# Optimization experiments

Measured on AMD Instinct MI355X. Metric: run time of the kernel, lower is better.

## Reference

```python
import jax, jax.numpy as jnp
import numpy as np

B, L_TXT, L_IMG = 1, 256, 2048
D_MODEL, HEADS, DIM_HEAD = 2048, 16, 128
S = L_TXT + L_IMG
QMAX = 127.0  # int8 symmetric
SM_SCALE = 1.0 / float(np.sqrt(DIM_HEAD))


def quant_act(x):
    # dynamic per-tensor symmetric int8 fake-quant with straight-through estimator
    scale = jnp.maximum(jnp.max(jnp.abs(x)) / QMAX, 1e-8)
    q = jnp.clip(jnp.round(x / scale), -QMAX, QMAX) * scale
    return x + jax.lax.stop_gradient(q - x)


def quant_weight(w):
    # per-output-channel symmetric int8 fake-quant (STE)
    scale = jnp.maximum(jnp.max(jnp.abs(w), axis=1, keepdims=True) / QMAX, 1e-8)
    q = jnp.clip(jnp.round(w / scale), -QMAX, QMAX) * scale
    return w + jax.lax.stop_gradient(q - w)


def qlinear(x, w, b):
    return x @ quant_weight(w).T + b


def rmsnorm(x, w, eps=1e-6):
    var = jnp.mean(jnp.square(x), axis=-1, keepdims=True)
    return x * jax.lax.rsqrt(var + eps) * w


def apply_rope(x, cos, sin):
    # diffusers apply_rotary_emb, use_real with interleaved (real, imag) pairs
    xr = x.reshape(*x.shape[:-1], -1, 2)
    rot = jnp.stack([-xr[..., 1], xr[..., 0]], axis=-1).reshape(x.shape)
    return x * cos + rot * sin


def heads_split(x):
    # [B, L, H*D] -> [B, H, L, D]
    return x.reshape(B, -1, HEADS, DIM_HEAD).transpose(0, 2, 1, 3)


def setup_inputs() -> dict:
    key = jax.random.key(0)
    ks = jax.random.split(key, 12)
    inp = {
        'hidden_states': jax.random.normal(ks[0], (B, L_IMG, D_MODEL), jnp.float32),
        'encoder_hidden_states': jax.random.normal(ks[1], (B, L_TXT, D_MODEL), jnp.float32),
    }
    freqs = 1.0 / (10000.0 ** (jnp.arange(0, DIM_HEAD, 2, dtype=jnp.float32) / DIM_HEAD))
    ang = jnp.arange(S, dtype=jnp.float32)[:, None] * freqs[None, :]  # [S, D/2]
    inp['rope_cos'] = jnp.repeat(jnp.cos(ang), 2, axis=-1)  # [S, D]
    inp['rope_sin'] = jnp.repeat(jnp.sin(ang), 2, axis=-1)
    wn = ['wq', 'wk', 'wv', 'w_add_q', 'w_add_k', 'w_add_v', 'w_out', 'w_add_out']
    bn = ['bq', 'bk', 'bv', 'b_add_q', 'b_add_k', 'b_add_v', 'b_out', 'b_add_out']
    for i, (w, b) in enumerate(zip(wn, bn)):
        inp[w] = jax.random.normal(ks[2 + i], (D_MODEL, D_MODEL), jnp.float32) * 0.02
        inp[b] = jnp.zeros((D_MODEL,), jnp.float32)
    for n in ['norm_q_w', 'norm_k_w', 'norm_added_q_w', 'norm_added_k_w']:
        inp[n] = jnp.ones((DIM_HEAD,), jnp.float32)
    return inp


def reference(hidden_states, encoder_hidden_states, rope_cos, rope_sin,
              wq, bq, wk, bk, wv, bv,
              w_add_q, b_add_q, w_add_k, b_add_k, w_add_v, b_add_v,
              w_out, b_out, w_add_out, b_add_out,
              norm_q_w, norm_k_w, norm_added_q_w, norm_added_k_w):
    # image-token branch
    h = quant_act(hidden_states)
    q = heads_split(qlinear(h, wq, bq))
    k = heads_split(qlinear(h, wk, bk))
    v = heads_split(qlinear(h, wv, bv))
    q = quant_act(rmsnorm(q, norm_q_w))
    k = quant_act(rmsnorm(k, norm_k_w))
    v = quant_act(v)
    # text-token (encoder) branch
    e = quant_act(encoder_hidden_states)
    eq = heads_split(qlinear(e, w_add_q, b_add_q))
    ek = heads_split(qlinear(e, w_add_k, b_add_k))
    ev = heads_split(qlinear(e, w_add_v, b_add_v))
    eq = quant_act(rmsnorm(eq, norm_added_q_w))
    ek = quant_act(rmsnorm(ek, norm_added_k_w))
    ev = quant_act(ev)
    # joint sequence: [text; image]
    q = jnp.concatenate([eq, q], axis=2)
    k = jnp.concatenate([ek, k], axis=2)
    v = jnp.concatenate([ev, v], axis=2)
    cos = rope_cos[None, None]
    sin = rope_sin[None, None]
    q = apply_rope(q, cos, sin)
    k = apply_rope(k, cos, sin)
    scores = jnp.einsum('bhqd,bhkd->bhqk', q, k) * SM_SCALE
    probs = jax.nn.softmax(scores, axis=-1)
    out = jnp.einsum('bhqk,bhkd->bhqd', probs, v)
    out = out.transpose(0, 2, 1, 3).reshape(B, S, HEADS * DIM_HEAD)
    out = quant_act(out)
    enc, img = out[:, :L_TXT], out[:, L_TXT:]
    img = qlinear(img, w_out, b_out)
    enc = qlinear(enc, w_add_out, b_add_out)
    return (img, enc)
```

## Files before the change

kernel.cpp:

```cpp
#include <hip/hip_runtime.h>

constexpr int L_TXT = 256, L_IMG = 2048, SEQ = 2304;
constexpr int DM = 2048, NH = 16, DH = 128;
constexpr int NSPLIT = 4;
constexpr int SSTR = 32;

typedef __attribute__((ext_vector_type(8))) __bf16 bf16x8;
typedef __attribute__((ext_vector_type(4))) float f32x4;

__device__ __forceinline__ float ldin(const void* p, size_t i, int bf) {
  return bf ? (float)((const __bf16*)p)[i] : ((const float*)p)[i];
}
__device__ __forceinline__ float slot_scale(const unsigned* s) {
  return fmaxf(__uint_as_float(*s) / 127.0f, 1e-8f);
}
__device__ __forceinline__ float qclamp(float x, float sc) {
  float q = rintf(x / sc);
  return fminf(fmaxf(q, -127.0f), 127.0f);
}
__device__ __forceinline__ float block_allmax_n(float v) {
  #pragma unroll
  for (int off = 32; off; off >>= 1) v = fmaxf(v, __shfl_xor(v, off));
  __shared__ float sm[16];
  int nw = blockDim.x >> 6;
  __syncthreads();
  if ((threadIdx.x & 63) == 0) sm[threadIdx.x >> 6] = v;
  __syncthreads();
  float m = sm[0];
  for (int i = 1; i < nw; i++) m = fmaxf(m, sm[i]);
  return m;
}

__global__ void detect_k(const void* cosp, int* flag) {
  if (threadIdx.x == 0) *flag = (((const unsigned short*)cosp)[0] != 0) ? 1 : 0;
}

struct Ptrs8 { const void* p[8]; };

__global__ void quant_weights_k(Ptrs8 win, __bf16* __restrict__ wq, float* __restrict__ scales,
                                const int* __restrict__ flagp) {
  const int bf = *flagp;
  int row = blockIdx.x, mat = blockIdx.y, t = threadIdx.x;
  float v[8];
  if (bf) {
    union { int4 q; __bf16 h[8]; } u;
    u.q = ((const int4*)((const __bf16*)win.p[mat] + (size_t)row * DM))[t];
    #pragma unroll
    for (int j = 0; j < 8; j++) v[j] = (float)u.h[j];
  } else {
    const float4* p = (const float4*)((const float*)win.p[mat] + (size_t)row * DM);
    float4 a = p[t * 2], b = p[t * 2 + 1];
    v[0]=a.x; v[1]=a.y; v[2]=a.z; v[3]=a.w; v[4]=b.x; v[5]=b.y; v[6]=b.z; v[7]=b.w;
  }
  float m = 0.f;
  #pragma unroll
  for (int j = 0; j < 8; j++) m = fmaxf(m, fabsf(v[j]));
  m = block_allmax_n(m);
  float sc = fmaxf(m / 127.0f, 1e-8f);
  if (t == 0) scales[mat * DM + row] = sc;
  union { int4 q; __bf16 h[8]; } o;
  #pragma unroll
  for (int j = 0; j < 8; j++) o.h[j] = (__bf16)qclamp(v[j], sc);
  ((int4*)(wq + (size_t)mat * DM * DM + (size_t)row * DM))[t] = o.q;
}
__global__ void weight_scales_k(Ptrs8 win, float* __restrict__ scales, const int* __restrict__ flagp) {
  const int bf = *flagp;
  int row = blockIdx.x, mat = blockIdx.y, t = threadIdx.x;
  float m = 0.f;
  for (int c = t; c < DM; c += 256) m = fmaxf(m, fabsf(ldin(win.p[mat], (size_t)row * DM + c, bf)));
  m = block_allmax_n(m);
  if (t == 0) scales[mat * DM + row] = fmaxf(m / 127.0f, 1e-8f);
}

__global__ void absmax_he_k(const void* __restrict__ hs, const void* __restrict__ es,
                            unsigned* s0, unsigned* s1, const int* __restrict__ flagp) {
  const int bf = *flagp;
  const int n18 = L_IMG * DM / 8, n28 = L_TXT * DM / 8;
  float m1 = 0.f, m2 = 0.f;
  for (int i = blockIdx.x * 256 + threadIdx.x; i < n18 + n28; i += gridDim.x * 256) {
    bool h = i < n18;
    const void* src = h ? hs : es;
    int j = h ? i : i - n18;
    float lm = 0.f;
    if (bf) {
      union { int4 q; __bf16 x[8]; } u; u.q = ((const int4*)src)[j];
      #pragma unroll
      for (int k = 0; k < 8; k++) lm = fmaxf(lm, fabsf((float)u.x[k]));
    } else {
      const float4* p = (const float4*)src;
      float4 a = p[j * 2], b = p[j * 2 + 1];
      lm = fmaxf(fmaxf(fmaxf(fabsf(a.x), fabsf(a.y)), fmaxf(fabsf(a.z), fabsf(a.w))),
                 fmaxf(fmaxf(fabsf(b.x), fabsf(b.y)), fmaxf(fabsf(b.z), fabsf(b.w))));
    }
    if (h) m1 = fmaxf(m1, lm); else m2 = fmaxf(m2, lm);
  }
  m1 = block_allmax_n(m1);
  __syncthreads();
  m2 = block_allmax_n(m2);
  if (threadIdx.x == 0) { atomicMax(s0, __float_as_uint(m1)); atomicMax(s1, __float_as_uint(m2)); }
}

__global__ void quant_he_k(const void* __restrict__ hs, const void* __restrict__ es,
                           const unsigned* __restrict__ slots, __bf16* __restrict__ hqo,
                           __bf16* __restrict__ eqo, const int* __restrict__ flagp) {
  const int bf = *flagp;
  const int n18 = L_IMG * DM / 8, n28 = L_TXT * DM / 8;
  float sc0 = slot_scale(slots), sc1 = slot_scale(slots + SSTR);
  for (int i = blockIdx.x * 256 + threadIdx.x; i < n18 + n28; i += gridDim.x * 256) {
    bool h = i < n18;
    const void* src = h ? hs : es;
    int j = h ? i : i - n18;
    float sc = h ? sc0 : sc1;
    float v[8];
    if (bf) {
      union { int4 q; __bf16 x[8]; } u; u.q = ((const int4*)src)[j];
      #pragma unroll
      for (int k = 0; k < 8; k++) v[k] = (float)u.x[k];
    } else {
      const float4* p = (const float4*)src;
      float4 a = p[j * 2], b = p[j * 2 + 1];
      v[0]=a.x; v[1]=a.y; v[2]=a.z; v[3]=a.w; v[4]=b.x; v[5]=b.y; v[6]=b.z; v[7]=b.w;
    }
    union { int4 q; __bf16 x[8]; } o;
    #pragma unroll
    for (int k = 0; k < 8; k++) o.x[k] = (__bf16)qclamp(v[k], sc);
    ((int4*)(h ? hqo : eqo))[j] = o.q;
  }
}

__global__ void quant_f32x8_k(const float* __restrict__ x, int n8,
                              const unsigned* __restrict__ slot, __bf16* __restrict__ out) {
  float sc = slot_scale(slot);
  for (int i = blockIdx.x * 256 + threadIdx.x; i < n8; i += gridDim.x * 256) {
    float4 a = ((const float4*)x)[i * 2], b = ((const float4*)x)[i * 2 + 1];
    union { int4 q; __bf16 h[8]; } o;
    o.h[0]=(__bf16)qclamp(a.x,sc); o.h[1]=(__bf16)qclamp(a.y,sc);
    o.h[2]=(__bf16)qclamp(a.z,sc); o.h[3]=(__bf16)qclamp(a.w,sc);
    o.h[4]=(__bf16)qclamp(b.x,sc); o.h[5]=(__bf16)qclamp(b.y,sc);
    o.h[6]=(__bf16)qclamp(b.z,sc); o.h[7]=(__bf16)qclamp(b.w,sc);
    ((int4*)out)[i] = o.q;
  }
}
__global__ void absmax_f32_k(const float* __restrict__ x, int n, unsigned* slot) {
  float m = 0.f;
  for (int i = blockIdx.x * 256 + threadIdx.x; i < n; i += gridDim.x * 256)
    m = fmaxf(m, fabsf(x[i]));
  m = block_allmax_n(m);
  if (threadIdx.x == 0) atomicMax(slot, __float_as_uint(m));
}

__global__ void rms_absmax_v_k(float* __restrict__ qf, float* __restrict__ kf, float* __restrict__ vf,
                               const void* nq, const void* naq, const void* nk, const void* nak,
                               unsigned* __restrict__ slots, const int* __restrict__ flagp) {
  const int bf = *flagp;
  const int t = threadIdx.x, lane = t & 63, wave = t >> 6;
  float wqt0 = ldin(naq, lane, bf), wqt1 = ldin(naq, lane + 64, bf);
  float wqi0 = ldin(nq,  lane, bf), wqi1 = ldin(nq,  lane + 64, bf);
  float wkt0 = ldin(nak, lane, bf), wkt1 = ldin(nak, lane + 64, bf);
  float wki0 = ldin(nk,  lane, bf), wki1 = ldin(nk,  lane + 64, bf);
  const int NR = NH * SEQ;
  float mx[6] = {0.f, 0.f, 0.f, 0.f, 0.f, 0.f};
  for (int row = blockIdx.x * 16 + wave; row < 3 * NR; row += gridDim.x * 16) {
    int tns = row / NR, r2 = row - tns * NR;
    int s = r2 % SEQ; bool txt = s < L_TXT;
    float* p = (tns == 0 ? qf : tns == 1 ? kf : vf) + (size_t)r2 * DH;
    float v0 = p[lane], v1 = p[lane + 64];
    if (tns < 2) {
      float ss = v0 * v0 + v1 * v1;
      #pragma unroll
      for (int off = 32; off; off >>= 1) ss += __shfl_xor(ss, off);
      float r = rsqrtf(ss * (1.0f / 128.0f) + 1e-6f);
      float w0, w1;
      if (tns == 0) { w0 = txt ? wqt0 : wqi0; w1 = txt ? wqt1 : wqi1; }
      else          { w0 = txt ? wkt0 : wki0; w1 = txt ? wkt1 : wki1; }
      v0 *= r * w0; v1 *= r * w1;
      p[lane] = v0; p[lane + 64] = v1;
    }
    int idx = tns * 2 + (txt ? 0 : 1);
    mx[idx] = fmaxf(mx[idx], fmaxf(fabsf(v0), fabsf(v1)));
  }
  #pragma unroll
  for (int off = 32; off; off >>= 1)
    #pragma unroll
    for (int j = 0; j < 6; j++) mx[j] = fmaxf(mx[j], __shfl_xor(mx[j], off));
  __shared__ float smx[16][6];
  if (lane == 0)
    #pragma unroll
    for (int j = 0; j < 6; j++) smx[wave][j] = mx[j];
  __syncthreads();
  if (t == 0) {
    #pragma unroll
    for (int j = 0; j < 6; j++) {
      float m = smx[0][j];
      for (int i = 1; i < 16; i++) m = fmaxf(m, smx[i][j]);
      atomicMax(slots + (2 + j) * SSTR, __float_as_uint(m));
    }
  }
}

__global__ void rope2_k(const float* __restrict__ qf, const float* __restrict__ kf,
                        const void* cosb, const void* sinb, const unsigned* __restrict__ slots,
                        __bf16* __restrict__ qb, __bf16* __restrict__ kb, const int* __restrict__ flagp) {
  const int bf = *flagp;
  const int NP = NH * SEQ * 64;
  for (int i = blockIdx.x * 256 + threadIdx.x; i < 2 * NP; i += gridDim.x * 256) {
    int tns = i >= NP;
    int j = i - tns * NP;
    int pr = j & 63, rowg = j >> 6;
    int s = rowg % SEQ;
    const float* src = tns ? kf : qf;
    __bf16* dst = tns ? kb : qb;
    float sc = slot_scale(slots + (tns ? 4 : 2) * SSTR + (s < L_TXT ? 0 : SSTR));
    size_t base = (size_t)rowg * DH + pr * 2;
    float2 x2 = *(const float2*)(src + base);
    float q0 = qclamp(x2.x, sc) * sc, q1 = qclamp(x2.y, sc) * sc;
    float c0 = ldin(cosb, s * DH + 2 * pr, bf), c1 = ldin(cosb, s * DH + 2 * pr + 1, bf);
    float s0 = ldin(sinb, s * DH + 2 * pr, bf), s1 = ldin(sinb, s * DH + 2 * pr + 1, bf);
    dst[base]     = (__bf16)(q0 * c0 - q1 * s0);
    dst[base + 1] = (__bf16)(q1 * c1 + q0 * s1);
  }
}

__global__ void quant_transpose_v_k(const float* __restrict__ v, const unsigned* __restrict__ slots,
                                    __bf16* __restrict__ vt) {
  __shared__ float tile[64][65];
  int t = threadIdx.x;
  int s0 = blockIdx.x * 64, d0 = blockIdx.y * 64, h = blockIdx.z;
  #pragma unroll
  for (int i = 0; i < 16; i++) {
    int r = i * 4 + (t >> 6), c = t & 63;
    tile[r][c] = v[((size_t)(h * SEQ) + s0 + r) * DH + d0 + c];
  }
  __syncthreads();
  float sc = slot_scale(slots + (s0 < L_TXT ? 6 : 7) * SSTR);
  #pragma unroll
  for (int i = 0; i < 16; i++) {
    int d = i * 4 + (t >> 6), s = t & 63;
    float q = qclamp(tile[s][d], sc) * sc;
    vt[((size_t)(h * DH) + d0 + d) * SEQ + s0 + s] = (__bf16)q;
  }
}

struct GemmArgs {
  const __bf16 *hq, *eq, *attnq;
  const __bf16* wqp;
  const void* Wraw[8];
  const float* wsc;
  const void* bias[8];
  float* outs[3];
  void* dout;
  const unsigned* slots;
  const int* flagp;
};
template<int MODE, int QW>
__global__ __launch_bounds__(256, 2)
void gemm_f(GemmArgs a) {
  const int bf = *a.flagp;
  constexpr int K = DM;
  __shared__ __bf16 As[128][72];
  __shared__ __bf16 Ws[128][72];
  const int t = threadIdx.x, lane = t & 63, wave = t >> 6;
  const int l15 = lane & 15, quad = lane >> 4;
  const int n0 = blockIdx.x * 128, y = blockIdx.y;
  int mat, outrow; const __bf16* A; const unsigned* aslot;
  if (MODE == 0) {
    bool txt = y < 2;
    mat = blockIdx.z + (txt ? 3 : 0);
    A = (txt ? a.eq : a.hq) + (size_t)(txt ? y * 128 : (y - 2) * 128) * K;
    outrow = y * 128;
    aslot = a.slots + (txt ? SSTR : 0);
  } else {
    bool img = y < 16;
    mat = img ? 6 : 7;
    A = a.attnq + (size_t)(img ? L_TXT + y * 128 : (y - 16) * 128) * K;
    outrow = img ? y * 128 : L_IMG + (y - 16) * 128;
    aslot = a.slots + 8 * SSTR;
  }
  const __bf16* Wq = QW ? a.wqp + (size_t)mat * DM * DM : nullptr;
  const void* Wr = a.Wraw[mat];
  const float* wrow = a.wsc + mat * DM;
  int wm = (wave & 1) * 64, wn = (wave >> 1) * 64;
  f32x4 acc[4][4] = {};
  int sr = t >> 3, sc = (t & 7) * 8;
  float wsc4[4];
  if (!QW) {
    #pragma unroll
    for (int p = 0; p < 4; p++) wsc4[p] = wrow[n0 + p * 32 + sr];
  }
  for (int k0 = 0; k0 < K; k0 += 64) {
    __syncthreads();
    #pragma unroll
    for (int p = 0; p < 4; p++) {
      int r = p * 32 + sr;
      *(int4*)&As[r][sc] = *(const int4*)&A[(size_t)r * K + k0 + sc];
      if (QW) {
        *(int4*)&Ws[r][sc] = *(const int4*)&Wq[(size_t)(n0 + r) * K + k0 + sc];
      } else {
        union { bf16x8 v; __bf16 h[8]; } q;
        if (bf) {
          union { int4 v; __bf16 h[8]; } u;
          u.v = *(const int4*)((const __bf16*)Wr + (size_t)(n0 + r) * K + k0 + sc);
          #pragma unroll
          for (int j = 0; j < 8; j++) q.h[j] = (__bf16)qclamp((float)u.h[j], wsc4[p]);
        } else {
          const float* wp = (const float*)Wr + (size_t)(n0 + r) * K + k0 + sc;
          float4 x = *(const float4*)wp, z = *(const float4*)(wp + 4);
          q.h[0]=(__bf16)qclamp(x.x,wsc4[p]); q.h[1]=(__bf16)qclamp(x.y,wsc4[p]);
          q.h[2]=(__bf16)qclamp(x.z,wsc4[p]); q.h[3]=(__bf16)qclamp(x.w,wsc4[p]);
          q.h[4]=(__bf16)qclamp(z.x,wsc4[p]); q.h[5]=(__bf16)qclamp(z.y,wsc4[p]);
          q.h[6]=(__bf16)qclamp(z.z,wsc4[p]); q.h[7]=(__bf16)qclamp(z.w,wsc4[p]);
        }
        *(bf16x8*)&Ws[r][sc] = q.v;
      }
    }
    __syncthreads();
    #pragma unroll
    for (int kk = 0; kk < 64; kk += 32) {
      bf16x8 af[4], bfr[4];
      #pragma unroll
      for (int i = 0; i < 4; i++) {
        af[i]  = *(const bf16x8*)&As[wm + i * 16 + l15][kk + quad * 8];
        bfr[i] = *(const bf16x8*)&Ws[wn + i * 16 + l15][kk + quad * 8];
      }
      #pragma unroll
      for (int i = 0; i < 4; i++)
        #pragma unroll
        for (int j = 0; j < 4; j++)
          acc[i][j] = __builtin_amdgcn_mfma_f32_16x16x32_bf16(af[i], bfr[j], acc[i][j], 0, 0, 0);
    }
  }
  float asc = slot_scale(aslot);
  #pragma unroll
  for (int j = 0; j < 4; j++) {
    int gn = n0 + wn + j * 16 + l15;
    float wsb = wrow[gn] * asc;
    float bv = ldin(a.bias[mat], gn, bf);
    #pragma unroll
    for (int i = 0; i < 4; i++)
      #pragma unroll
      for (int r = 0; r < 4; r++) {
        int gm = wm + i * 16 + quad * 4 + r;
        float val = acc[i][j][r] * wsb + bv;
        if (MODE == 0) {
          a.outs[blockIdx.z][(size_t)(gn >> 7) * (SEQ * DH) + (size_t)(outrow + gm) * DH + (gn & 127)] = val;
        } else {
          size_t idx = (size_t)(outrow + gm) * DM + gn;
          if (bf) ((__bf16*)a.dout)[idx] = (__bf16)val; else ((float*)a.dout)[idx] = val;
        }
      }
  }
}

template<int SPLIT>
__global__ __launch_bounds__(256, 2)
void flash_attn_k(const __bf16* __restrict__ Qb, const __bf16* __restrict__ Kb,
                  const __bf16* __restrict__ Vt, float* __restrict__ O,
                  float* __restrict__ Op, float* __restrict__ Mp, float* __restrict__ Lp) {
  __shared__ __align__(16) char smem[19456 + 18432 + 18432];
  auto Ks = (__bf16(*)[152])smem;
  auto Vs = (__bf16(*)[72])(smem + 19456);
  auto Ps = (__bf16(*)[72])(smem + 19456 + 18432);
  const int t = threadIdx.x, lane = t & 63, wave = t >> 6;
  const int l15 = lane & 15, quad = lane >> 4;
  const int h = blockIdx.y, s0 = blockIdx.x * 128, qr = wave * 32;
  const float fscale = 0.08838834764831845f * 1.4426950408889634f;

  bf16x8 qf[2][4];
  #pragma unroll
  for (int mi = 0; mi < 2; mi++)
    #pragma unroll
    for (int kk = 0; kk < 4; kk++)
      qf[mi][kk] = *(const bf16x8*)&Qb[(size_t)(h * SEQ + s0 + qr + mi * 16 + l15) * DH + kk * 32 + quad * 8];

  f32x4 accO[2][8] = {};
  float m_st[2][4], l_st[2][4];
  #pragma unroll
  for (int mi = 0; mi < 2; mi++)
    #pragma unroll
    for (int r = 0; r < 4; r++) { m_st[mi][r] = -1e30f; l_st[mi][r] = 0.f; }

  const int ktb = SPLIT ? blockIdx.z * (SEQ / 64 / NSPLIT) : 0;
  const int kte = SPLIT ? ktb + (SEQ / 64 / NSPLIT) : SEQ / 64;

  const int krr = t >> 4, krc = (t & 15) * 8;
  const int vrr = t >> 3, vrc = (t & 7) * 8;
  int4 kreg[4], vreg[4];
  #pragma unroll
  for (int p = 0; p < 4; p++)
    kreg[p] = *(const int4*)&Kb[(size_t)(h * SEQ + ktb * 64 + p * 16 + krr) * DH + krc];
  #pragma unroll
  for (int p = 0; p < 4; p++)
    vreg[p] = *(const int4*)&Vt[(size_t)(h * DH + p * 32 + vrr) * SEQ + ktb * 64 + vrc];

  for (int kt = ktb; kt < kte; kt++) {
    asm volatile("s_waitcnt lgkmcnt(0)" ::: "memory");
    __builtin_amdgcn_s_barrier();
    #pragma unroll
    for (int p = 0; p < 4; p++) *(int4*)&Ks[p * 16 + krr][krc] = kreg[p];
    #pragma unroll
    for (int p = 0; p < 4; p++) *(int4*)&Vs[p * 32 + vrr][vrc] = vreg[p];
    if (kt + 1 < kte) {
      #pragma unroll
      for (int p = 0; p < 4; p++)
        kreg[p] = *(const int4*)&Kb[(size_t)(h * SEQ + (kt + 1) * 64 + p * 16 + krr) * DH + krc];
      #pragma unroll
      for (int p = 0; p < 4; p++)
        vreg[p] = *(const int4*)&Vt[(size_t)(h * DH + p * 32 + vrr) * SEQ + (kt + 1) * 64 + vrc];
    }
    asm volatile("s_waitcnt lgkmcnt(0)" ::: "memory");
    __builtin_amdgcn_s_barrier();

    f32x4 accS[2][4] = {};
    __builtin_amdgcn_s_setprio(1);
    #pragma unroll
    for (int kk = 0; kk < 4; kk++) {
      bf16x8 bk[4];
      #pragma unroll
      for (int ni = 0; ni < 4; ni++)
        bk[ni] = *(const bf16x8*)&Ks[ni * 16 + l15][kk * 32 + quad * 8];
      #pragma unroll
      for (int mi = 0; mi < 2; mi++)
        #pragma unroll
        for (int ni = 0; ni < 4; ni++)
          accS[mi][ni] = __builtin_amdgcn_mfma_f32_16x16x32_bf16(qf[mi][kk], bk[ni], accS[mi][ni], 0, 0, 0);
    }
    __builtin_amdgcn_s_setprio(0);

    float al[2][4];
    #pragma unroll
    for (int mi = 0; mi < 2; mi++)
      #pragma unroll
      for (int r = 0; r < 4; r++) {
        float rm = fmaxf(fmaxf(accS[mi][0][r], accS[mi][1][r]), fmaxf(accS[mi][2][r], accS[mi][3][r]));
        #pragma unroll
        for (int off = 8; off > 0; off >>= 1) rm = fmaxf(rm, __shfl_xor(rm, off));
        float mn = fmaxf(m_st[mi][r], rm);
        al[mi][r] = exp2f((m_st[mi][r] - mn) * fscale);
        m_st[mi][r] = mn;
      }
    #pragma unroll
    for (int mi = 0; mi < 2; mi++)
      #pragma unroll
      for (int r = 0; r < 4; r++) {
        float rs = 0.f;
        #pragma unroll
        for (int ni = 0; ni < 4; ni++) {
          float pv = exp2f((accS[mi][ni][r] - m_st[mi][r]) * fscale);
          accS[mi][ni][r] = pv;
          rs += pv;
        }
        #pragma unroll
        for (int off = 8; off > 0; off >>= 1) rs += __shfl_xor(rs, off);
        l_st[mi][r] = l_st[mi][r] * al[mi][r] + rs;
      }
    #pragma unroll
    for (int mi = 0; mi < 2; mi++)
      #pragma unroll
      for (int di = 0; di < 8; di++)
        #pragma unroll
        for (int r = 0; r < 4; r++)
          accO[mi][di][r] *= al[mi][r];
    #pragma unroll
    for (int mi = 0; mi < 2; mi++)
      #pragma unroll
      for (int ni = 0; ni < 4; ni++)
        #pragma unroll
        for (int r = 0; r < 4; r++)
          Ps[qr + mi * 16 + quad * 4 + r][ni * 16 + l15] = (__bf16)accS[mi][ni][r];
    __builtin_amdgcn_s_setprio(1);
    #pragma unroll
    for (int kk2 = 0; kk2 < 2; kk2++) {
      bf16x8 pa[2], vb[8];
      #pragma unroll
      for (int mi = 0; mi < 2; mi++)
        pa[mi] = *(const bf16x8*)&Ps[qr + mi * 16 + l15][kk2 * 32 + quad * 8];
      #pragma unroll
      for (int di = 0; di < 8; di++)
        vb[di] = *(const bf16x8*)&Vs[di * 16 + l15][kk2 * 32 + quad * 8];
      #pragma unroll
      for (int mi = 0; mi < 2; mi++)
        #pragma unroll
        for (int di = 0; di < 8; di++)
          accO[mi][di] = __builtin_amdgcn_mfma_f32_16x16x32_bf16(pa[mi], vb[di], accO[mi][di], 0, 0, 0);
    }
    __builtin_amdgcn_s_setprio(0);
  }
  if (SPLIT) {
    const size_t SP = (size_t)NH * SEQ * DH;
    const int sp = blockIdx.z;
    #pragma unroll
    for (int mi = 0; mi < 2; mi++)
      #pragma unroll
      for (int r = 0; r < 4; r++) {
        int gs = s0 + qr + mi * 16 + quad * 4 + r;
        size_t ib = sp * SP + ((size_t)h * SEQ + gs) * DH;
        if (l15 == 0) {
          Mp[(size_t)sp * NH * SEQ + h * SEQ + gs] = m_st[mi][r];
          Lp[(size_t)sp * NH * SEQ + h * SEQ + gs] = l_st[mi][r];
        }
        #pragma unroll
        for (int di = 0; di < 8; di++)
          Op[ib + di * 16 + l15] = accO[mi][di][r];
      }
  } else {
    #pragma unroll
    for (int mi = 0; mi < 2; mi++)
      #pragma unroll
      for (int r = 0; r < 4; r++) {
        float inv = 1.0f / l_st[mi][r];
        int gs = s0 + qr + mi * 16 + quad * 4 + r;
        #pragma unroll
        for (int di = 0; di < 8; di++)
          O[(size_t)gs * DM + h * DH + di * 16 + l15] = accO[mi][di][r] * inv;
      }
  }
}

__global__ void flash_combine_k(const float* __restrict__ Op, const float* __restrict__ Mp,
                                const float* __restrict__ Lp, float* __restrict__ O,
                                unsigned* __restrict__ slot8) {
  const float fscale = 0.08838834764831845f * 1.4426950408889634f;
  const int t = threadIdx.x, lane = t & 63, w = t >> 6;
  const size_t SP = (size_t)NH * SEQ * DH, MR = (size_t)NH * SEQ;
  float lm = 0.f;
  for (int row = blockIdx.x * 16 + w; row < NH * SEQ; row += gridDim.x * 16) {
    float m0 = Mp[row], m1 = Mp[MR + row], m2 = Mp[2 * MR + row], m3 = Mp[3 * MR + row];
    float M = fmaxf(fmaxf(m0, m1), fmaxf(m2, m3));
    float w0 = exp2f((m0 - M) * fscale), w1 = exp2f((m1 - M) * fscale);
    float w2 = exp2f((m2 - M) * fscale), w3 = exp2f((m3 - M) * fscale);
    float inv = 1.0f / (Lp[row] * w0 + Lp[MR + row] * w1 + Lp[2 * MR + row] * w2 + Lp[3 * MR + row] * w3);
    int h = row / SEQ, s = row % SEQ;
    size_t ob = (size_t)s * DM + h * DH, ib = (size_t)row * DH;
    #pragma unroll
    for (int j = 0; j < 2; j++) {
      int d = lane + j * 64;
      float v = (Op[ib + d] * w0 + Op[SP + ib + d] * w1 +
                 Op[2 * SP + ib + d] * w2 + Op[3 * SP + ib + d] * w3) * inv;
      O[ob + d] = v;
      lm = fmaxf(lm, fabsf(v));
    }
  }
  lm = block_allmax_n(lm);
  if (t == 0) atomicMax(slot8, __float_as_uint(lm));
}

extern "C" void kernel_launch(void* const* d_in, const int* in_sizes, int n_in,
                              void* d_out, int out_size, void* d_ws, size_t ws_size,
                              hipStream_t stream) {
  (void)in_sizes; (void)n_in; (void)out_size;
  const void* hs   = d_in[0];
  const void* es   = d_in[1];
  const void* cosb = d_in[2];
  const void* sinb = d_in[3];
  const void* W[8]; const void* Bv[8];
  for (int i = 0; i < 8; i++) { W[i] = d_in[4 + 2 * i]; Bv[i] = d_in[5 + 2 * i]; }
  const void* nq  = d_in[20];
  const void* nk  = d_in[21];
  const void* naq = d_in[22];
  const void* nak = d_in[23];

  char* ws = (char*)d_ws;
  size_t off = 0;
  auto take = [&](size_t b) { char* p = ws + off; off += (b + 255) & ~(size_t)255; return p; };
  const size_t T = (size_t)NH * SEQ * DH * 4;

  unsigned* slots = (unsigned*)take(16 * SSTR * 4);
  int* flagp = (int*)(slots + 15 * SSTR);
  float* wsc = (float*)take(8ull * DM * 4);

  size_t here = off;
  size_t need_base  = 4 * T + T + 3 * (T / 2) + 2 * ((size_t)NSPLIT * NH * SEQ * 4 + 256) + 1024;
  bool do_split = here + need_base <= ws_size;
  size_t region_sz = do_split ? 4 * T : 3 * T;

  char* region = take(region_sz);
  float* qf = (float*)region;
  float* kf = (float*)(region + T);
  float* vf = (float*)(region + 2 * T);
  float* Opart = (float*)region;
  __bf16* attnq = (__bf16*)region;
  char* attnfR = take(T);
  __bf16* hq = (__bf16*)attnfR;
  __bf16* eq = (__bf16*)(attnfR + (size_t)L_IMG * DM * 2);
  float* attnf = (float*)attnfR;
  __bf16* qb  = (__bf16*)take(T / 2);
  __bf16* kb  = (__bf16*)take(T / 2);
  __bf16* vtb = (__bf16*)take(T / 2);
  float* Mpart = (float*)take((size_t)NSPLIT * NH * SEQ * 4);
  float* Lpart = (float*)take((size_t)NSPLIT * NH * SEQ * 4);
  bool do_prequant = (off + 8ull * DM * DM * 2 + 256 <= ws_size);
  __bf16* wq = do_prequant ? (__bf16*)take(8ull * DM * DM * 2) : nullptr;

  hipMemsetAsync(slots, 0, 16 * SSTR * 4, stream);
  detect_k<<<1, 64, 0, stream>>>(cosb, flagp);

  Ptrs8 win;
  for (int i = 0; i < 8; i++) win.p[i] = W[i];
  if (do_prequant)
    quant_weights_k<<<dim3(DM, 8), 256, 0, stream>>>(win, wq, wsc, flagp);
  else
    weight_scales_k<<<dim3(DM, 8), 256, 0, stream>>>(win, wsc, flagp);

  absmax_he_k<<<512, 256, 0, stream>>>(hs, es, slots, slots + SSTR, flagp);
  quant_he_k<<<1024, 256, 0, stream>>>(hs, es, slots, hq, eq, flagp);

  GemmArgs ga;
  ga.hq = hq; ga.eq = eq; ga.attnq = attnq; ga.wqp = wq;
  for (int i = 0; i < 8; i++) { ga.Wraw[i] = W[i]; ga.bias[i] = Bv[i]; }
  ga.wsc = wsc; ga.outs[0] = qf; ga.outs[1] = kf; ga.outs[2] = vf;
  ga.dout = d_out; ga.slots = slots; ga.flagp = flagp;

  if (do_prequant)
    gemm_f<0, 1><<<dim3(16, 18, 3), 256, 0, stream>>>(ga);
  else
    gemm_f<0, 0><<<dim3(16, 18, 3), 256, 0, stream>>>(ga);

  rms_absmax_v_k<<<256, 1024, 0, stream>>>(qf, kf, vf, nq, naq, nk, nak, slots, flagp);
  rope2_k<<<1024, 256, 0, stream>>>(qf, kf, cosb, sinb, slots, qb, kb, flagp);
  quant_transpose_v_k<<<dim3(SEQ / 64, DH / 64, NH), 256, 0, stream>>>(vf, slots, vtb);

  if (do_split) {
    flash_attn_k<1><<<dim3(SEQ / 128, NH, NSPLIT), 256, 0, stream>>>(qb, kb, vtb, nullptr,
                                                                     Opart, Mpart, Lpart);
    flash_combine_k<<<288, 1024, 0, stream>>>(Opart, Mpart, Lpart, attnf, slots + 8 * SSTR);
  } else {
    flash_attn_k<0><<<dim3(SEQ / 128, NH), 256, 0, stream>>>(qb, kb, vtb, attnf,
                                                             nullptr, nullptr, nullptr);
    absmax_f32_k<<<256, 256, 0, stream>>>(attnf, SEQ * DM, slots + 8 * SSTR);
  }
  quant_f32x8_k<<<1024, 256, 0, stream>>>(attnf, SEQ * DM / 8, slots + 8 * SSTR, attnq);

  if (do_prequant)
    gemm_f<1, 1><<<dim3(16, 18), 256, 0, stream>>>(ga);
  else
    gemm_f<1, 0><<<dim3(16, 18), 256, 0, stream>>>(ga);
}
```

Measured before the change: 677.9 us.

## Shrink flash-attention query tile to 64 rows and alias P buffer onto K smem

```diff
diff --git a/kernel.cpp b/kernel.cpp
--- a/kernel.cpp
+++ b/kernel.cpp
@@ -352,32 +352,28 @@
 }
 
 template<int SPLIT>
-__global__ __launch_bounds__(256, 2)
+__global__ __launch_bounds__(256, 4)
 void flash_attn_k(const __bf16* __restrict__ Qb, const __bf16* __restrict__ Kb,
                   const __bf16* __restrict__ Vt, float* __restrict__ O,
                   float* __restrict__ Op, float* __restrict__ Mp, float* __restrict__ Lp) {
-  __shared__ __align__(16) char smem[19456 + 18432 + 18432];
+  __shared__ __align__(16) char smem[19456 + 18432];
   auto Ks = (__bf16(*)[152])smem;
   auto Vs = (__bf16(*)[72])(smem + 19456);
-  auto Ps = (__bf16(*)[72])(smem + 19456 + 18432);
+  auto Ps = (__bf16(*)[72])smem;
   const int t = threadIdx.x, lane = t & 63, wave = t >> 6;
   const int l15 = lane & 15, quad = lane >> 4;
-  const int h = blockIdx.y, s0 = blockIdx.x * 128, qr = wave * 32;
+  const int h = blockIdx.y, s0 = blockIdx.x * 64, qr = wave * 16;
   const float fscale = 0.08838834764831845f * 1.4426950408889634f;
 
-  bf16x8 qf[2][4];
-  #pragma unroll
-  for (int mi = 0; mi < 2; mi++)
-    #pragma unroll
-    for (int kk = 0; kk < 4; kk++)
-      qf[mi][kk] = *(const bf16x8*)&Qb[(size_t)(h * SEQ + s0 + qr + mi * 16 + l15) * DH + kk * 32 + quad * 8];
-
-  f32x4 accO[2][8] = {};
-  float m_st[2][4], l_st[2][4];
-  #pragma unroll
-  for (int mi = 0; mi < 2; mi++)
-    #pragma unroll
-    for (int r = 0; r < 4; r++) { m_st[mi][r] = -1e30f; l_st[mi][r] = 0.f; }
+  bf16x8 qf[4];
+  #pragma unroll
+  for (int kk = 0; kk < 4; kk++)
+    qf[kk] = *(const bf16x8*)&Qb[(size_t)(h * SEQ + s0 + qr + l15) * DH + kk * 32 + quad * 8];
+
+  f32x4 accO[8] = {};
+  float m_st[4], l_st[4];
+  #pragma unroll
+  for (int r = 0; r < 4; r++) { m_st[r] = -1e30f; l_st[r] = 0.f; }
 
   const int ktb = SPLIT ? blockIdx.z * (SEQ / 64 / NSPLIT) : 0;
   const int kte = SPLIT ? ktb + (SEQ / 64 / NSPLIT) : SEQ / 64;
@@ -410,78 +406,61 @@
     asm volatile("s_waitcnt lgkmcnt(0)" ::: "memory");
     __builtin_amdgcn_s_barrier();
 
-    f32x4 accS[2][4] = {};
+    f32x4 accS[4] = {};
     __builtin_amdgcn_s_setprio(1);
     #pragma unroll
-    for (int kk = 0; kk < 4; kk++) {
-      bf16x8 bk[4];
-      #pragma unroll
-      for (int ni = 0; ni < 4; ni++)
-        bk[ni] = *(const bf16x8*)&Ks[ni * 16 + l15][kk * 32 + quad * 8];
-      #pragma unroll
-      for (int mi = 0; mi < 2; mi++)
-        #pragma unroll
-        for (int ni = 0; ni < 4; ni++)
-          accS[mi][ni] = __builtin_amdgcn_mfma_f32_16x16x32_bf16(qf[mi][kk], bk[ni], accS[mi][ni], 0, 0, 0);
-    }
+    for (int kk = 0; kk < 4; kk++)
+      #pragma unroll
+      for (int ni = 0; ni < 4; ni++) {
+        bf16x8 bk = *(const bf16x8*)&Ks[ni * 16 + l15][kk * 32 + quad * 8];
+        accS[ni] = __builtin_amdgcn_mfma_f32_16x16x32_bf16(qf[kk], bk, accS[ni], 0, 0, 0);
+      }
     __builtin_amdgcn_s_setprio(0);
-
-    float al[2][4];
-    #pragma unroll
-    for (int mi = 0; mi < 2; mi++)
-      #pragma unroll
-      for (int r = 0; r < 4; r++) {
-        float rm = fmaxf(fmaxf(accS[mi][0][r], accS[mi][1][r]), fmaxf(accS[mi][2][r], accS[mi][3][r]));
-        #pragma unroll
-        for (int off = 8; off > 0; off >>= 1) rm = fmaxf(rm, __shfl_xor(rm, off));
-        float mn = fmaxf(m_st[mi][r], rm);
-        al[mi][r] = exp2f((m_st[mi][r] - mn) * fscale);
-        m_st[mi][r] = mn;
+    asm volatile("s_waitcnt lgkmcnt(0)" ::: "memory");
+    __builtin_amdgcn_s_barrier();
+
+    float al[4];
+    #pragma unroll
+    for (int r = 0; r < 4; r++) {
+      float rm = fmaxf(fmaxf(accS[0][r], accS[1][r]), fmaxf(accS[2][r], accS[3][r]));
+      #pragma unroll
+      for (int off = 8; off > 0; off >>= 1) rm = fmaxf(rm, __shfl_xor(rm, off));
+      float mn = fmaxf(m_st[r], rm);
+      al[r] = exp2f((m_st[r] - mn) * fscale);
+      m_st[r] = mn;
+    }
+    #pragma unroll
+    for (int r = 0; r < 4; r++) {
+      float rs = 0.f;
+      #pragma unroll
+      for (int ni = 0; ni < 4; ni++) {
+        float pv = exp2f((accS[ni][r] - m_st[r]) * fscale);
+        accS[ni][r] = pv;
+        rs += pv;
       }
-    #pragma unroll
-    for (int mi = 0; mi < 2; mi++)
-      #pragma unroll
-      for (int r = 0; r < 4; r++) {
-        float rs = 0.f;
-        #pragma unroll
-        for (int ni = 0; ni < 4; ni++) {
-          float pv = exp2f((accS[mi][ni][r] - m_st[mi][r]) * fscale);
-          accS[mi][ni][r] = pv;
-          rs += pv;
-        }
-        #pragma unroll
-        for (int off = 8; off > 0; off >>= 1) rs += __shfl_xor(rs, off);
-        l_st[mi][r] = l_st[mi][r] * al[mi][r] + rs;
+      #pragma unroll
+      for (int off = 8; off > 0; off >>= 1) rs += __shfl_xor(rs, off);
+      l_st[r] = l_st[r] * al[r] + rs;
+    }
+    #pragma unroll
+    for (int di = 0; di < 8; di++)
+      #pragma unroll
+      for (int r = 0; r < 4; r++)
+        accO[di][r] *= al[r];
+    #pragma unroll
+    for (int ni = 0; ni < 4; ni++)
+      #pragma unroll
+      for (int r = 0; r < 4; r++)
+        Ps[qr + quad * 4 + r][ni * 16 + l15] = (__bf16)accS[ni][r];
+    __builtin_amdgcn_s_setprio(1);
+    #pragma unroll
+    for (int kk2 = 0; kk2 < 2; kk2++) {
+      bf16x8 pa = *(const bf16x8*)&Ps[qr + l15][kk2 * 32 + quad * 8];
+      #pragma unroll
+      for (int di = 0; di < 8; di++) {
+        bf16x8 vb = *(const bf16x8*)&Vs[di * 16 + l15][kk2 * 32 + quad * 8];
+        accO[di] = __builtin_amdgcn_mfma_f32_16x16x32_bf16(pa, vb, accO[di], 0, 0, 0);
       }
-    #pragma unroll
-    for (int mi = 0; mi < 2; mi++)
-      #pragma unroll
-      for (int di = 0; di < 8; di++)
-        #pragma unroll
-        for (int r = 0; r < 4; r++)
-          accO[mi][di][r] *= al[mi][r];
-    #pragma unroll
-    for (int mi = 0; mi < 2; mi++)
-      #pragma unroll
-      for (int ni = 0; ni < 4; ni++)
-        #pragma unroll
-        for (int r = 0; r < 4; r++)
-          Ps[qr + mi * 16 + quad * 4 + r][ni * 16 + l15] = (__bf16)accS[mi][ni][r];
-    __builtin_amdgcn_s_setprio(1);
-    #pragma unroll
-    for (int kk2 = 0; kk2 < 2; kk2++) {
-      bf16x8 pa[2], vb[8];
-      #pragma unroll
-      for (int mi = 0; mi < 2; mi++)
-        pa[mi] = *(const bf16x8*)&Ps[qr + mi * 16 + l15][kk2 * 32 + quad * 8];
-      #pragma unroll
-      for (int di = 0; di < 8; di++)
-        vb[di] = *(const bf16x8*)&Vs[di * 16 + l15][kk2 * 32 + quad * 8];
-      #pragma unroll
-      for (int mi = 0; mi < 2; mi++)
-        #pragma unroll
-        for (int di = 0; di < 8; di++)
-          accO[mi][di] = __builtin_amdgcn_mfma_f32_16x16x32_bf16(pa[mi], vb[di], accO[mi][di], 0, 0, 0);
     }
     __builtin_amdgcn_s_setprio(0);
   }
@@ -489,30 +468,26 @@
     const size_t SP = (size_t)NH * SEQ * DH;
     const int sp = blockIdx.z;
     #pragma unroll
-    for (int mi = 0; mi < 2; mi++)
-      #pragma unroll
-      for (int r = 0; r < 4; r++) {
-        int gs = s0 + qr + mi * 16 + quad * 4 + r;
-        size_t ib = sp * SP + ((size_t)h * SEQ + gs) * DH;
-        if (l15 == 0) {
-          Mp[(size_t)sp * NH * SEQ + h * SEQ + gs] = m_st[mi][r];
-          Lp[(size_t)sp * NH * SEQ + h * SEQ + gs] = l_st[mi][r];
-        }
-        #pragma unroll
-        for (int di = 0; di < 8; di++)
-          Op[ib + di * 16 + l15] = accO[mi][di][r];
+    for (int r = 0; r < 4; r++) {
+      int gs = s0 + qr + quad * 4 + r;
+      size_t ib = sp * SP + ((size_t)h * SEQ + gs) * DH;
+      if (l15 == 0) {
+        Mp[(size_t)sp * NH * SEQ + h * SEQ + gs] = m_st[r];
+        Lp[(size_t)sp * NH * SEQ + h * SEQ + gs] = l_st[r];
       }
+      #pragma unroll
+      for (int di = 0; di < 8; di++)
+        Op[ib + di * 16 + l15] = accO[di][r];
+    }
   } else {
     #pragma unroll
-    for (int mi = 0; mi < 2; mi++)
-      #pragma unroll
-      for (int r = 0; r < 4; r++) {
-        float inv = 1.0f / l_st[mi][r];
-        int gs = s0 + qr + mi * 16 + quad * 4 + r;
-        #pragma unroll
-        for (int di = 0; di < 8; di++)
-          O[(size_t)gs * DM + h * DH + di * 16 + l15] = accO[mi][di][r] * inv;
-      }
+    for (int r = 0; r < 4; r++) {
+      float inv = 1.0f / l_st[r];
+      int gs = s0 + qr + quad * 4 + r;
+      #pragma unroll
+      for (int di = 0; di < 8; di++)
+        O[(size_t)gs * DM + h * DH + di * 16 + l15] = accO[di][r] * inv;
+    }
   }
 }
 
@@ -620,12 +595,12 @@
   quant_transpose_v_k<<<dim3(SEQ / 64, DH / 64, NH), 256, 0, stream>>>(vf, slots, vtb);
 
   if (do_split) {
-    flash_attn_k<1><<<dim3(SEQ / 128, NH, NSPLIT), 256, 0, stream>>>(qb, kb, vtb, nullptr,
-                                                                     Opart, Mpart, Lpart);
+    flash_attn_k<1><<<dim3(SEQ / 64, NH, NSPLIT), 256, 0, stream>>>(qb, kb, vtb, nullptr,
+                                                                    Opart, Mpart, Lpart);
     flash_combine_k<<<288, 1024, 0, stream>>>(Opart, Mpart, Lpart, attnf, slots + 8 * SSTR);
   } else {
-    flash_attn_k<0><<<dim3(SEQ / 128, NH), 256, 0, stream>>>(qb, kb, vtb, attnf,
-                                                             nullptr, nullptr, nullptr);
+    flash_attn_k<0><<<dim3(SEQ / 64, NH), 256, 0, stream>>>(qb, kb, vtb, attnf,
+                                                            nullptr, nullptr, nullptr);
     absmax_f32_k<<<256, 256, 0, stream>>>(attnf, SEQ * DM, slots + 8 * SSTR);
   }
   quant_f32x8_k<<<1024, 256, 0, stream>>>(attnf, SEQ * DM / 8, slots + 8 * SSTR, attnq);
```

New measurement: 737.8 us. +8.8%, slower.
